# Optimization experiments

Hardware: AMD Instinct MI355X
Metric: run time of the kernel (lower is better)

## Reference

```python
import jax, jax.numpy as jnp
import numpy as np

HEADS = 16
D_MODEL = 1024
D_EXP = 2048  # d_model * expansion_factor
D_HEAD = D_EXP // HEADS
DEPTH = 12
B, L = 2, 2048


def setup_inputs() -> dict:
    key = jax.random.key(0)
    ks = jax.random.split(key, 4)
    x = jax.random.normal(ks[0], (B, L, D_MODEL), dtype=jnp.float32)
    w_in = jax.random.normal(ks[1], (4 * D_EXP, D_MODEL), dtype=jnp.float32) * 0.02
    w_out = jax.random.normal(ks[2], (D_MODEL, D_EXP), dtype=jnp.float32) * (0.02 / np.sqrt(2 * DEPTH))
    # LearnedALiBi init: logspace(0,-6,heads//2,base=2) ++ zeros(heads - heads//2)
    half = HEADS // 2
    slopes = jnp.concatenate([
        jnp.asarray(2.0 ** np.linspace(0.0, -6.0, half), dtype=jnp.float32),
        jnp.zeros((HEADS - half,), dtype=jnp.float32),
    ])
    smear_factor = jnp.linspace(-6.0, 6.0, HEADS, dtype=jnp.float32)
    return {
        "x": x, "w_in": w_in, "w_out": w_out,
        "ln_in_g": jnp.ones((D_MODEL,), jnp.float32), "ln_in_b": jnp.zeros((D_MODEL,), jnp.float32),
        "ln_out_g": jnp.ones((D_MODEL,), jnp.float32), "ln_out_b": jnp.zeros((D_MODEL,), jnp.float32),
        "slopes": slopes, "smear_factor": smear_factor,
    }


def _layernorm(x, g, b, eps=1e-5):
    mu = jnp.mean(x, axis=-1, keepdims=True)
    var = jnp.mean(jnp.square(x - mu), axis=-1, keepdims=True)
    return (x - mu) * jax.lax.rsqrt(var + eps) * g + b


def reference(x, w_in, w_out, ln_in_g, ln_in_b, ln_out_g, ln_out_b, slopes, smear_factor):
    b, l, d = x.shape
    h = _layernorm(x, ln_in_g, ln_in_b)
    qkvp = h @ w_in.T  # (b, l, 4*D_EXP)
    q, k, v, p = jnp.split(qkvp, 4, axis=-1)

    def to_heads(t):  # b i (h d) -> b h i d
        return t.reshape(b, l, HEADS, D_HEAD).transpose(0, 2, 1, 3)

    q, k, v = to_heads(q), to_heads(k), to_heads(v)

    # key smearing: k_i <- (1-s)*k_i + s*k_{i-1}
    smear = jax.nn.sigmoid(smear_factor)[None, :, None, None]
    k_shift = jnp.pad(k, ((0, 0), (0, 0), (1, 0), (0, 0)))[:, :, :-1]
    k = (1.0 - smear) * k + smear * k_shift

    logits = jnp.einsum('bhid,bhjd->bhij', q, k) * (D_HEAD ** -0.5)
    # learned ALiBi bias: j * slope_h  (depends only on key index)
    alibi = jnp.arange(l, dtype=logits.dtype)[None, None, None, :] * slopes[None, :, None, None]
    # causal bias: -1e10 * (1 - tril)
    i_idx = jnp.arange(l)
    causal = jnp.where(i_idx[:, None] >= i_idx[None, :], 0.0, -1e10)[None, None]
    a = jax.nn.softmax(logits + alibi + causal, axis=-1)

    o = jnp.einsum('bhij,bhjd->bhid', a, v)
    o = o.transpose(0, 2, 1, 3).reshape(b, l, D_EXP)  # b h i d -> b i (h d)
    gated = jax.nn.silu(p) * o
    y = gated @ w_out.T
    return _layernorm(y, ln_out_g, ln_out_b)
```

## Files before the change

kernel.cpp:

```cpp
#include <hip/hip_runtime.h>
#include <hip/hip_bf16.h>
#include <stdint.h>


typedef __bf16 bf16;
typedef bf16  bf16x8 __attribute__((ext_vector_type(8)));
typedef bf16  bf16x4 __attribute__((ext_vector_type(4)));
typedef float f32x4  __attribute__((ext_vector_type(4)));

#define SEQ   2048
#define NBATC 2

__device__ __forceinline__ void gld_lds16(const bf16* g, bf16* l) {
  __builtin_amdgcn_global_load_lds((const __attribute__((address_space(1))) void*)g,
                                   (__attribute__((address_space(3))) void*)l, 16, 0, 0);
}

__global__ __launch_bounds__(256) void cvt_kernel(const float* __restrict__ in,
                                                  bf16* __restrict__ out, int n8) {
  int t = blockIdx.x * 256 + threadIdx.x;
  if (t >= n8) return;
  const float4* p = (const float4*)in + (size_t)t * 2;
  float4 a = p[0], b = p[1];
  bf16x8 o;
  o[0] = (bf16)a.x; o[1] = (bf16)a.y; o[2] = (bf16)a.z; o[3] = (bf16)a.w;
  o[4] = (bf16)b.x; o[5] = (bf16)b.y; o[6] = (bf16)b.z; o[7] = (bf16)b.w;
  *((bf16x8*)out + t) = o;
}

template<bool BF16OUT>
__global__ __launch_bounds__(256) void ln_kernel(const float* __restrict__ x,
    const float* __restrict__ gamma, const float* __restrict__ beta,
    void* __restrict__ out) {
  const int row = blockIdx.x;
  const int tid = threadIdx.x;
  float4 v = *(const float4*)(x + (size_t)row * 1024 + tid * 4);
  float s  = v.x + v.y + v.z + v.w;
  float ss = v.x * v.x + v.y * v.y + v.z * v.z + v.w * v.w;
#pragma unroll
  for (int m = 1; m < 64; m <<= 1) { s += __shfl_xor(s, m, 64); ss += __shfl_xor(ss, m, 64); }
  __shared__ float red[8];
  if ((tid & 63) == 0) { red[tid >> 6] = s; red[(tid >> 6) + 4] = ss; }
  __syncthreads();
  s  = red[0] + red[1] + red[2] + red[3];
  ss = red[4] + red[5] + red[6] + red[7];
  const float mu  = s * (1.f / 1024.f);
  const float inv = rsqrtf(ss * (1.f / 1024.f) - mu * mu + 1e-5f);
  float4 g  = *(const float4*)(gamma + tid * 4);
  float4 bb = *(const float4*)(beta  + tid * 4);
  float y0 = (v.x - mu) * inv * g.x + bb.x;
  float y1 = (v.y - mu) * inv * g.y + bb.y;
  float y2 = (v.z - mu) * inv * g.z + bb.z;
  float y3 = (v.w - mu) * inv * g.w + bb.w;
  if (BF16OUT) {
    bf16* o = (bf16*)out + (size_t)row * 1024 + tid * 4;
    o[0] = (bf16)y0; o[1] = (bf16)y1; o[2] = (bf16)y2; o[3] = (bf16)y3;
  } else {
    float* o = (float*)out + (size_t)row * 1024 + tid * 4;
    o[0] = y0; o[1] = y1; o[2] = y2; o[3] = y3;
  }
}

__global__ __launch_bounds__(256) void prep_kernel(const bf16* __restrict__ qkvp,
    const float* __restrict__ smf, bf16* __restrict__ ksm, bf16* __restrict__ vt) {
  __shared__ bf16 T[128][72];
  const int kt = blockIdx.x, bh = blockIdx.y;
  const int b = bh >> 4, h = bh & 15;
  const int t = threadIdx.x;

  {
    int i = t >> 2, d0 = (t & 3) * 32;
    const bf16* src = qkvp + (size_t)(b * SEQ + kt * 64 + i) * 8192 + 4096 + h * 128 + d0;
#pragma unroll
    for (int m = 0; m < 4; m++) {
      bf16x8 v8 = *(const bf16x8*)(src + m * 8);
#pragma unroll
      for (int e = 0; e < 8; e++) T[d0 + m * 8 + e][i] = v8[e];
    }
  }

  {
    float sm = 1.f / (1.f + __expf(-smf[h]));
#pragma unroll
    for (int j = 0; j < 4; j++) {
      int c  = j * 256 + t;
      int il = c >> 4, d8 = c & 15;
      int i  = kt * 64 + il;
      const bf16* base = qkvp + (size_t)(b * SEQ + i) * 8192 + 2048 + h * 128 + d8 * 8;
      bf16x8 cur = *(const bf16x8*)base;
      bf16x8 prv = cur;
      if (i > 0) prv = *(const bf16x8*)(base - 8192);
      bf16x8 o;
#pragma unroll
      for (int e = 0; e < 8; e++) {
        float pv = (i > 0) ? (float)prv[e] : 0.f;
        o[e] = (bf16)((1.f - sm) * (float)cur[e] + sm * pv);
      }
      size_t idx = ((size_t)bh * SEQ + i) * 128 + ((d8 * 8) ^ ((i & 7) << 3));
      *(bf16x8*)(ksm + idx) = o;
    }
  }

  __syncthreads();
  {
    int d = t >> 1, i0 = (t & 1) * 32;
    bf16* dst = vt + (size_t)bh * (SEQ * 128) + (size_t)kt * 8192 + d * 64;
#pragma unroll
    for (int m = 0; m < 4; m++) {
      bf16x8 v8 = *(const bf16x8*)&T[d][i0 + m * 8];
      *(bf16x8*)(dst + (((i0 + m * 8)) ^ ((d & 7) << 3))) = v8;
    }
  }
}

__global__ __launch_bounds__(512, 2) void gemm256(const bf16* __restrict__ A,
    const bf16* __restrict__ Bt, bf16* __restrict__ C, int M, int N, int K,
    int RX, int SX, int SY) {
  __shared__ bf16 As[2][2][128 * 64];
  __shared__ bf16 Bs[2][2][128 * 64];
  const int w   = blockIdx.x;
  const int xcd = w & 7, idx = w >> 3;
  const int rx = xcd % RX, ry = xcd / RX;
  const int bx = rx * SX + idx % SX;
  const int by = ry * SY + idx / SX;
  const int tid  = threadIdx.x;
  const int lane = tid & 63, wid = tid >> 6;
  const int l4 = lane >> 4, l16 = lane & 15;
  const int wr = wid >> 2, wc = wid & 3;
  const int rowBase = by * 256, colBase = bx * 256;
  const int NT = K >> 6;

  f32x4 acc[8][4];
  const f32x4 z = {0.f, 0.f, 0.f, 0.f};
#pragma unroll
  for (int i = 0; i < 8; i++)
#pragma unroll
    for (int j = 0; j < 4; j++) acc[i][j] = z;

  auto stage_pair = [&](int t_, int hp) {
    const int buf = t_ & 1, k0 = t_ * 64;
#pragma unroll
    for (int half = 0; half < 2; ++half) {
      const bf16* src = (hp == 0) ? (A  + (size_t)(rowBase + half * 128) * K)
                                  : (Bt + (size_t)(colBase + half * 128) * K);
      bf16* dst = (hp == 0) ? &As[buf][half][0] : &Bs[buf][half][0];
#pragma unroll
      for (int j = 0; j < 2; ++j) {
        const int c   = j * 512 + tid;
        const int row = c >> 3;
        const int sc  = ((c & 7) * 8) ^ ((row & 7) << 3);
        gld_lds16(src + (size_t)row * K + k0 + sc, dst + c * 8);
      }
    }
  };

  stage_pair(0, 0);
  stage_pair(0, 1);
  asm volatile("s_waitcnt vmcnt(0)" ::: "memory");
  __builtin_amdgcn_sched_barrier(0);
  __builtin_amdgcn_s_barrier();

  for (int t = 0; t < NT; ++t) {
    const int buf = t & 1;
    const bf16* aH = &As[buf][wr][0];
    const bf16* bH = &Bs[buf][wc >> 1][0];
    bf16x8 bfr[4];
#pragma unroll
    for (int p = 0; p < 4; ++p) {
      const int ks = p >> 1, mh = p & 1;
      bf16x8 af[4];
#pragma unroll
      for (int q = 0; q < 4; ++q) {
        const int lr = mh * 64 + q * 16 + l16;
        af[q] = *(const bf16x8*)&aH[lr * 64 + ((ks * 32 + l4 * 8) ^ ((lr & 7) << 3))];
      }
      if (mh == 0) {
#pragma unroll
        for (int ni = 0; ni < 4; ++ni) {
          const int lr = (wc & 1) * 64 + ni * 16 + l16;
          bfr[ni] = *(const bf16x8*)&bH[lr * 64 + ((ks * 32 + l4 * 8) ^ ((lr & 7) << 3))];
        }
      }
      if (p == 0 && t + 1 < NT) stage_pair(t + 1, 0);
      if (p == 1 && t + 1 < NT) stage_pair(t + 1, 1);
      __builtin_amdgcn_s_barrier();
      asm volatile("s_waitcnt lgkmcnt(0)" ::: "memory");
      __builtin_amdgcn_sched_barrier(0);
      __builtin_amdgcn_s_setprio(1);
#pragma unroll
      for (int q = 0; q < 4; ++q)
#pragma unroll
        for (int ni = 0; ni < 4; ++ni)
          acc[mh * 4 + q][ni] =
              __builtin_amdgcn_mfma_f32_16x16x32_bf16(af[q], bfr[ni], acc[mh * 4 + q][ni], 0, 0, 0);
      __builtin_amdgcn_s_setprio(0);
      if (p == 3) {
        asm volatile("s_waitcnt vmcnt(0)" ::: "memory");
        __builtin_amdgcn_sched_barrier(0);
      }
      __builtin_amdgcn_s_barrier();
    }
  }

#pragma unroll
  for (int mi = 0; mi < 8; ++mi)
#pragma unroll
    for (int ni = 0; ni < 4; ++ni) {
      int row = rowBase + wr * 128 + mi * 16 + l4 * 4;
      int col = colBase + wc * 64 + ni * 16 + l16;
#pragma unroll
      for (int r = 0; r < 4; ++r)
        C[(size_t)(row + r) * N + col] = (bf16)acc[mi][ni][r];
    }
}

template<typename OutT>
__global__ __launch_bounds__(256) void gemm_bt(const bf16* __restrict__ A,
    const bf16* __restrict__ Bt, OutT* __restrict__ C, int M, int N, int K,
    int RX, int SX, int SY) {
  __shared__ bf16 As[128 * 32];
  __shared__ bf16 Bs[128 * 32];
  const int w   = blockIdx.x;
  const int xcd = w & 7, idx = w >> 3;
  const int rx = xcd % RX, ry = xcd / RX;
  const int bx = rx * SX + idx % SX;
  const int by = ry * SY + idx / SX;
  const int tid  = threadIdx.x;
  const int lane = tid & 63, wid = tid >> 6;
  const int l4 = lane >> 4, l16 = lane & 15;
  const int wr = wid >> 1, wc = wid & 1;
  const int rowBase = by * 128, colBase = bx * 128;

  const bf16* gA = A  + (size_t)(rowBase + (tid >> 2)) * K + (tid & 3) * 8;
  const bf16* gB = Bt + (size_t)(colBase + (tid >> 2)) * K + (tid & 3) * 8;
  const size_t rowStep = (size_t)64 * K;

  f32x4 acc[4][4];
  const f32x4 z = {0.f, 0.f, 0.f, 0.f};
#pragma unroll
  for (int i = 0; i < 4; i++)
#pragma unroll
    for (int j = 0; j < 4; j++) acc[i][j] = z;

  for (int k0 = 0; k0 < K; k0 += 32) {
    __syncthreads();
    gld_lds16(gA + k0,           &As[tid * 8]);
    gld_lds16(gA + rowStep + k0, &As[2048 + tid * 8]);
    gld_lds16(gB + k0,           &Bs[tid * 8]);
    gld_lds16(gB + rowStep + k0, &Bs[2048 + tid * 8]);
    __syncthreads();
    bf16x8 af[4], bfr[4];
#pragma unroll
    for (int mi = 0; mi < 4; mi++)
      af[mi] = *(const bf16x8*)&As[(wr * 64 + mi * 16 + l16) * 32 + l4 * 8];
#pragma unroll
    for (int ni = 0; ni < 4; ni++)
      bfr[ni] = *(const bf16x8*)&Bs[(wc * 64 + ni * 16 + l16) * 32 + l4 * 8];
#pragma unroll
    for (int mi = 0; mi < 4; mi++)
#pragma unroll
      for (int ni = 0; ni < 4; ni++)
        acc[mi][ni] = __builtin_amdgcn_mfma_f32_16x16x32_bf16(af[mi], bfr[ni], acc[mi][ni], 0, 0, 0);
  }
#pragma unroll
  for (int mi = 0; mi < 4; mi++)
#pragma unroll
    for (int ni = 0; ni < 4; ni++) {
      int row = rowBase + wr * 64 + mi * 16 + l4 * 4;
      int col = colBase + wc * 64 + ni * 16 + l16;
#pragma unroll
      for (int r = 0; r < 4; r++)
        C[(size_t)(row + r) * N + col] = (OutT)acc[mi][ni][r];
    }
}

__global__ __launch_bounds__(512, 2) void attn_kernel(const bf16* __restrict__ qkvp,
    const bf16* __restrict__ ksm, const bf16* __restrict__ vt,
    const float* __restrict__ slopes, bf16* __restrict__ gated) {
  const int w   = blockIdx.x;
  const int xcd = w & 7;
  const int bh  = xcd * 4 + ((w >> 3) & 3);
  const int pr  = w >> 5;
  const int b   = bh >> 4, h = bh & 15;
  const int tid = threadIdx.x, wid = tid >> 6, lane = tid & 63;
  const int l4 = lane >> 4, l16 = lane & 15;
  const int swz = (l16 & 7) << 3;
  const float LOG2E = 1.44269504f;
  const float s2 = 0.08838834764831845f * LOG2E;
  const float slopeL = slopes[h] * LOG2E;

  __shared__ bf16 Kb[4][64 * 128];
  __shared__ bf16 Vb[4][64 * 128];
  __shared__ bf16 P_lds[128 * 64];

  const bf16* ksmB = ksm + (size_t)bh * SEQ * 128;
  const bf16* vtB  = vt  + (size_t)bh * SEQ * 128;

  auto stage = [&](int kt, int bsel) {
#pragma unroll
    for (int j = 0; j < 2; j++) {
      const int c = j * 512 + tid;
      gld_lds16(ksmB + (size_t)kt * 8192 + c * 8, &Kb[bsel][c * 8]);
      gld_lds16(vtB  + (size_t)kt * 8192 + c * 8, &Vb[bsel][c * 8]);
    }
  };

  auto run_strip = [&](int qtile) {
    const int nt = 2 * qtile + 2;
    const int iq = qtile * 128 + wid * 16 + l16;
    bf16x8 qf[4];
    {
      const bf16* qrow = qkvp + (size_t)(b * SEQ + iq) * 8192 + h * 128;
#pragma unroll
      for (int kb = 0; kb < 4; kb++) qf[kb] = *(const bf16x8*)(qrow + kb * 32 + l4 * 8);
    }
    f32x4 oacc[8];
    const f32x4 z = {0.f, 0.f, 0.f, 0.f};
#pragma unroll
    for (int i = 0; i < 8; i++) oacc[i] = z;
    float m2 = -1e38f, lpart = 0.f;

    auto tile = [&](int t, const bf16* K_, const bf16* V_) {
      f32x4 sacc[4];
#pragma unroll
      for (int jf = 0; jf < 4; jf++) {
        f32x4 a = z;
#pragma unroll
        for (int kb = 0; kb < 4; kb++) {
          bf16x8 kf = *(const bf16x8*)&K_[(jf * 16 + l16) * 128 + ((kb * 32 + l4 * 8) ^ swz)];
          a = __builtin_amdgcn_mfma_f32_16x16x32_bf16(kf, qf[kb], a, 0, 0, 0);
        }
        sacc[jf] = a;
      }

      const bool diag = (t >= 2 * qtile);
      const int kbase = t * 64 + l4 * 4;
#pragma unroll
      for (int jf = 0; jf < 4; jf++) {
#pragma unroll
        for (int r = 0; r < 4; r++) {
          int j = kbase + jf * 16 + r;
          float v = fmaf(sacc[jf][r], s2, (float)j * slopeL);
          if (diag && j > iq) v = -1e38f;
          sacc[jf][r] = v;
        }
      }

      float mx = sacc[0][0];
#pragma unroll
      for (int jf = 0; jf < 4; jf++)
#pragma unroll
        for (int r = 0; r < 4; r++) mx = fmaxf(mx, sacc[jf][r]);
      mx = fmaxf(mx, __shfl_xor(mx, 16, 64));
      mx = fmaxf(mx, __shfl_xor(mx, 32, 64));

      if (__any(mx > m2 + 14.f)) {
        float mnew  = fmaxf(m2, mx);
        float alpha = __builtin_amdgcn_exp2f(m2 - mnew);
        m2 = mnew;
        lpart *= alpha;
#pragma unroll
        for (int df = 0; df < 8; df++) oacc[df] *= alpha;
      }

      float rs = 0.f;
#pragma unroll
      for (int jf = 0; jf < 4; jf++) {
        bf16x4 pw;
#pragma unroll
        for (int r = 0; r < 4; r++) {
          float pe = __builtin_amdgcn_exp2f(sacc[jf][r] - m2);
          rs += pe;
          pw[r] = (bf16)pe;
        }
        *(bf16x4*)&P_lds[(wid * 16 + l16) * 64 + ((jf * 16 + l4 * 4) ^ swz)] = pw;
      }
      lpart += rs;

#pragma unroll
      for (int kb2 = 0; kb2 < 2; ++kb2) {
        bf16x8 pf = *(const bf16x8*)&P_lds[(wid * 16 + l16) * 64 + ((kb2 * 32 + l4 * 8) ^ swz)];
#pragma unroll
        for (int df = 0; df < 8; df++) {
          bf16x8 vf = *(const bf16x8*)&V_[(df * 16 + l16) * 64 + ((kb2 * 32 + l4 * 8) ^ swz)];
          oacc[df] = __builtin_amdgcn_mfma_f32_16x16x32_bf16(vf, pf, oacc[df], 0, 0, 0);
        }
      }
    };

    stage(0, 0);
    stage(1, 1);
    for (int tp = 0; tp < nt; tp += 2) {
      if (tp + 2 < nt) {
        stage(tp + 2, (tp + 2) & 3);
        stage(tp + 3, (tp + 3) & 3);
        asm volatile("s_waitcnt vmcnt(8)" ::: "memory");
      } else {
        asm volatile("s_waitcnt vmcnt(0)" ::: "memory");
      }
      __builtin_amdgcn_sched_barrier(0);
      __builtin_amdgcn_s_barrier();
      tile(tp,     Kb[tp & 3],       Vb[tp & 3]);
      tile(tp + 1, Kb[(tp + 1) & 3], Vb[(tp + 1) & 3]);
      asm volatile("s_waitcnt lgkmcnt(0)" ::: "memory");
      __builtin_amdgcn_s_barrier();
    }

    lpart += __shfl_xor(lpart, 16, 64);
    lpart += __shfl_xor(lpart, 32, 64);
    const float linv = 1.f / lpart;
    const bf16* pgrow = qkvp + (size_t)(b * SEQ + iq) * 8192 + 6144 + h * 128;
    bf16* grow = gated + (size_t)(b * SEQ + iq) * 2048 + h * 128;
#pragma unroll
    for (int df = 0; df < 8; df++) {
      const int d0 = df * 16 + l4 * 4;
      bf16x4 pg4 = *(const bf16x4*)(pgrow + d0);
      bf16x4 o4;
#pragma unroll
      for (int r = 0; r < 4; r++) {
        float o  = oacc[df][r] * linv;
        float pg = (float)pg4[r];
        float silu = pg / (1.f + __expf(-pg));
        o4[r] = (bf16)(silu * o);
      }
      *(bf16x4*)(grow + d0) = o4;
    }
  };

  run_strip(15 - pr);
  run_strip(pr);
}

extern "C" void kernel_launch(void* const* d_in, const int* in_sizes, int n_in,
                              void* d_out, int out_size, void* d_ws, size_t ws_size,
                              hipStream_t stream) {
  (void)in_sizes; (void)n_in; (void)out_size; (void)ws_size;
  const float* x      = (const float*)d_in[0];
  const float* w_in   = (const float*)d_in[1];
  const float* w_out  = (const float*)d_in[2];
  const float* lnig   = (const float*)d_in[3];
  const float* lnib   = (const float*)d_in[4];
  const float* lnog   = (const float*)d_in[5];
  const float* lnob   = (const float*)d_in[6];
  const float* slopes = (const float*)d_in[7];
  const float* smf    = (const float*)d_in[8];
  float* out = (float*)d_out;

  char* ws = (char*)d_ws;
  size_t off = 0;
  bf16* hb      = (bf16*)(ws + off); off += (size_t)4096 * 1024 * 2;
  bf16* w_in_b  = (bf16*)(ws + off); off += (size_t)8192 * 1024 * 2;
  bf16* w_out_b = (bf16*)(ws + off); off += (size_t)1024 * 2048 * 2;
  bf16* qkvp    = (bf16*)(ws + off); off += (size_t)4096 * 8192 * 2;
  bf16* ksm     = (bf16*)(ws + off); off += (size_t)32 * 2048 * 128 * 2;
  bf16* gated   = (bf16*)(ws + off); off += (size_t)4096 * 2048 * 2;
  float* yb     = (float*)(ws + off); off += (size_t)4096 * 1024 * 4;
  bf16* vt      = (bf16*)yb;

  cvt_kernel<<<4096, 256, 0, stream>>>(w_in,  w_in_b,  8388608 / 8);
  cvt_kernel<<<1024, 256, 0, stream>>>(w_out, w_out_b, 2097152 / 8);
  ln_kernel<true><<<4096, 256, 0, stream>>>(x, lnig, lnib, hb);
  gemm256<<<512, 512, 0, stream>>>(hb, w_in_b, qkvp, 4096, 8192, 1024, 4, 8, 8);
  prep_kernel<<<dim3(32, 32), 256, 0, stream>>>(qkvp, smf, ksm, vt);
  attn_kernel<<<256, 512, 0, stream>>>(qkvp, ksm, vt, slopes, gated);
  gemm_bt<float><<<256, 256, 0, stream>>>(gated, w_out_b, yb, 4096, 1024, 2048, 1, 8, 4);
  ln_kernel<false><<<4096, 256, 0, stream>>>(yb, lnog, lnob, out);
}
```

Measured before the change: 229.1 us.

## Double-buffer output GEMM, share K/V tiles across attention strips, merge staging

The output projection GEMM is replaced by a double-buffered version with 64-wide K tiles and swizzled LDS, so global loads overlap the MFMA work instead of sitting between syncthreads. The attention kernel now processes its two query strips together, so each K/V tile loaded for the long strip is reused by the short strip rather than streamed twice. The big input GEMM issues both staging halves at the first sub-step. The cost is more registers (two sets of Q fragments and accumulators) and more LDS in the GEMM, which may lower occupancy.

```diff
diff --git a/kernel.cpp b/kernel.cpp
--- a/kernel.cpp
+++ b/kernel.cpp
@@ -181,8 +181,10 @@
           bfr[ni] = *(const bf16x8*)&bH[lr * 64 + ((ks * 32 + l4 * 8) ^ ((lr & 7) << 3))];
         }
       }
-      if (p == 0 && t + 1 < NT) stage_pair(t + 1, 0);
-      if (p == 1 && t + 1 < NT) stage_pair(t + 1, 1);
+      if (p == 0 && t + 1 < NT) {
+        stage_pair(t + 1, 0);
+        stage_pair(t + 1, 1);
+      }
       __builtin_amdgcn_s_barrier();
       asm volatile("s_waitcnt lgkmcnt(0)" ::: "memory");
       __builtin_amdgcn_sched_barrier(0);
@@ -214,12 +216,11 @@
     }
 }
 
-template<typename OutT>
-__global__ __launch_bounds__(256) void gemm_bt(const bf16* __restrict__ A,
-    const bf16* __restrict__ Bt, OutT* __restrict__ C, int M, int N, int K,
+__global__ __launch_bounds__(256, 2) void gemm128(const bf16* __restrict__ A,
+    const bf16* __restrict__ Bt, float* __restrict__ C, int M, int N, int K,
     int RX, int SX, int SY) {
-  __shared__ bf16 As[128 * 32];
-  __shared__ bf16 Bs[128 * 32];
+  __shared__ bf16 As[2][128 * 64];
+  __shared__ bf16 Bs[2][128 * 64];
   const int w   = blockIdx.x;
   const int xcd = w & 7, idx = w >> 3;
   const int rx = xcd % RX, ry = xcd / RX;
@@ -230,10 +231,7 @@
   const int l4 = lane >> 4, l16 = lane & 15;
   const int wr = wid >> 1, wc = wid & 1;
   const int rowBase = by * 128, colBase = bx * 128;
-
-  const bf16* gA = A  + (size_t)(rowBase + (tid >> 2)) * K + (tid & 3) * 8;
-  const bf16* gB = Bt + (size_t)(colBase + (tid >> 2)) * K + (tid & 3) * 8;
-  const size_t rowStep = (size_t)64 * K;
+  const int NT = K >> 6;
 
   f32x4 acc[4][4];
   const f32x4 z = {0.f, 0.f, 0.f, 0.f};
@@ -242,35 +240,61 @@
 #pragma unroll
     for (int j = 0; j < 4; j++) acc[i][j] = z;
 
-  for (int k0 = 0; k0 < K; k0 += 32) {
-    __syncthreads();
-    gld_lds16(gA + k0,           &As[tid * 8]);
-    gld_lds16(gA + rowStep + k0, &As[2048 + tid * 8]);
-    gld_lds16(gB + k0,           &Bs[tid * 8]);
-    gld_lds16(gB + rowStep + k0, &Bs[2048 + tid * 8]);
-    __syncthreads();
-    bf16x8 af[4], bfr[4];
-#pragma unroll
-    for (int mi = 0; mi < 4; mi++)
-      af[mi] = *(const bf16x8*)&As[(wr * 64 + mi * 16 + l16) * 32 + l4 * 8];
-#pragma unroll
-    for (int ni = 0; ni < 4; ni++)
-      bfr[ni] = *(const bf16x8*)&Bs[(wc * 64 + ni * 16 + l16) * 32 + l4 * 8];
-#pragma unroll
-    for (int mi = 0; mi < 4; mi++)
-#pragma unroll
-      for (int ni = 0; ni < 4; ni++)
-        acc[mi][ni] = __builtin_amdgcn_mfma_f32_16x16x32_bf16(af[mi], bfr[ni], acc[mi][ni], 0, 0, 0);
-  }
-#pragma unroll
-  for (int mi = 0; mi < 4; mi++)
-#pragma unroll
-    for (int ni = 0; ni < 4; ni++) {
+  auto stage = [&](int t_, int buf) {
+    const int k0 = t_ * 64;
+#pragma unroll
+    for (int j = 0; j < 4; ++j) {
+      const int c   = j * 256 + tid;
+      const int row = c >> 3;
+      const int sc  = ((c & 7) * 8) ^ ((row & 7) << 3);
+      gld_lds16(A  + (size_t)(rowBase + row) * K + k0 + sc, &As[buf][c * 8]);
+      gld_lds16(Bt + (size_t)(colBase + row) * K + k0 + sc, &Bs[buf][c * 8]);
+    }
+  };
+
+  stage(0, 0);
+  for (int t = 0; t < NT; ++t) {
+    const int cur = t & 1;
+    if (t + 1 < NT) {
+      stage(t + 1, cur ^ 1);
+      asm volatile("s_waitcnt vmcnt(8)" ::: "memory");
+    } else {
+      asm volatile("s_waitcnt vmcnt(0)" ::: "memory");
+    }
+    __builtin_amdgcn_sched_barrier(0);
+    __builtin_amdgcn_s_barrier();
+    const bf16* a_ = &As[cur][0];
+    const bf16* b_ = &Bs[cur][0];
+#pragma unroll
+    for (int ks = 0; ks < 2; ++ks) {
+      bf16x8 bfr[4];
+#pragma unroll
+      for (int ni = 0; ni < 4; ++ni) {
+        const int br = wc * 64 + ni * 16 + l16;
+        bfr[ni] = *(const bf16x8*)&b_[br * 64 + ((ks * 32 + l4 * 8) ^ ((br & 7) << 3))];
+      }
+#pragma unroll
+      for (int mi = 0; mi < 4; ++mi) {
+        const int ar = wr * 64 + mi * 16 + l16;
+        bf16x8 af = *(const bf16x8*)&a_[ar * 64 + ((ks * 32 + l4 * 8) ^ ((ar & 7) << 3))];
+#pragma unroll
+        for (int ni = 0; ni < 4; ++ni)
+          acc[mi][ni] = __builtin_amdgcn_mfma_f32_16x16x32_bf16(af, bfr[ni], acc[mi][ni], 0, 0, 0);
+      }
+    }
+    asm volatile("s_waitcnt lgkmcnt(0)" ::: "memory");
+    __builtin_amdgcn_s_barrier();
+  }
+
+#pragma unroll
+  for (int mi = 0; mi < 4; ++mi)
+#pragma unroll
+    for (int ni = 0; ni < 4; ++ni) {
       int row = rowBase + wr * 64 + mi * 16 + l4 * 4;
       int col = colBase + wc * 64 + ni * 16 + l16;
 #pragma unroll
-      for (int r = 0; r < 4; r++)
-        C[(size_t)(row + r) * N + col] = (OutT)acc[mi][ni][r];
+      for (int r = 0; r < 4; ++r)
+        C[(size_t)(row + r) * N + col] = acc[mi][ni][r];
     }
 }
 
@@ -281,6 +305,9 @@
   const int xcd = w & 7;
   const int bh  = xcd * 4 + ((w >> 3) & 3);
   const int pr  = w >> 5;
+  const int qtA = 15 - pr, qtB = pr;
+  const int ntA = 32 - 2 * pr;
+  const int ntB = 2 * pr + 2;
   const int b   = bh >> 4, h = bh & 15;
   const int tid = threadIdx.x, wid = tid >> 6, lane = tid & 63;
   const int l4 = lane >> 4, l16 = lane & 15;
@@ -305,107 +332,116 @@
     }
   };
 
-  auto run_strip = [&](int qtile) {
-    const int nt = 2 * qtile + 2;
-    const int iq = qtile * 128 + wid * 16 + l16;
-    bf16x8 qf[4];
-    {
-      const bf16* qrow = qkvp + (size_t)(b * SEQ + iq) * 8192 + h * 128;
-#pragma unroll
-      for (int kb = 0; kb < 4; kb++) qf[kb] = *(const bf16x8*)(qrow + kb * 32 + l4 * 8);
-    }
-    f32x4 oacc[8];
-    const f32x4 z = {0.f, 0.f, 0.f, 0.f};
-#pragma unroll
-    for (int i = 0; i < 8; i++) oacc[i] = z;
-    float m2 = -1e38f, lpart = 0.f;
-
-    auto tile = [&](int t, const bf16* K_, const bf16* V_) {
-      f32x4 sacc[4];
-#pragma unroll
-      for (int jf = 0; jf < 4; jf++) {
-        f32x4 a = z;
-#pragma unroll
-        for (int kb = 0; kb < 4; kb++) {
-          bf16x8 kf = *(const bf16x8*)&K_[(jf * 16 + l16) * 128 + ((kb * 32 + l4 * 8) ^ swz)];
-          a = __builtin_amdgcn_mfma_f32_16x16x32_bf16(kf, qf[kb], a, 0, 0, 0);
-        }
-        sacc[jf] = a;
-      }
-
-      const bool diag = (t >= 2 * qtile);
-      const int kbase = t * 64 + l4 * 4;
-#pragma unroll
-      for (int jf = 0; jf < 4; jf++) {
-#pragma unroll
-        for (int r = 0; r < 4; r++) {
-          int j = kbase + jf * 16 + r;
-          float v = fmaf(sacc[jf][r], s2, (float)j * slopeL);
-          if (diag && j > iq) v = -1e38f;
-          sacc[jf][r] = v;
-        }
-      }
-
-      float mx = sacc[0][0];
-#pragma unroll
-      for (int jf = 0; jf < 4; jf++)
-#pragma unroll
-        for (int r = 0; r < 4; r++) mx = fmaxf(mx, sacc[jf][r]);
-      mx = fmaxf(mx, __shfl_xor(mx, 16, 64));
-      mx = fmaxf(mx, __shfl_xor(mx, 32, 64));
-
-      if (__any(mx > m2 + 14.f)) {
-        float mnew  = fmaxf(m2, mx);
-        float alpha = __builtin_amdgcn_exp2f(m2 - mnew);
-        m2 = mnew;
-        lpart *= alpha;
-#pragma unroll
-        for (int df = 0; df < 8; df++) oacc[df] *= alpha;
-      }
-
-      float rs = 0.f;
-#pragma unroll
-      for (int jf = 0; jf < 4; jf++) {
-        bf16x4 pw;
-#pragma unroll
-        for (int r = 0; r < 4; r++) {
-          float pe = __builtin_amdgcn_exp2f(sacc[jf][r] - m2);
-          rs += pe;
-          pw[r] = (bf16)pe;
-        }
-        *(bf16x4*)&P_lds[(wid * 16 + l16) * 64 + ((jf * 16 + l4 * 4) ^ swz)] = pw;
-      }
-      lpart += rs;
-
-#pragma unroll
-      for (int kb2 = 0; kb2 < 2; ++kb2) {
-        bf16x8 pf = *(const bf16x8*)&P_lds[(wid * 16 + l16) * 64 + ((kb2 * 32 + l4 * 8) ^ swz)];
-#pragma unroll
-        for (int df = 0; df < 8; df++) {
-          bf16x8 vf = *(const bf16x8*)&V_[(df * 16 + l16) * 64 + ((kb2 * 32 + l4 * 8) ^ swz)];
-          oacc[df] = __builtin_amdgcn_mfma_f32_16x16x32_bf16(vf, pf, oacc[df], 0, 0, 0);
-        }
-      }
-    };
-
-    stage(0, 0);
-    stage(1, 1);
-    for (int tp = 0; tp < nt; tp += 2) {
-      if (tp + 2 < nt) {
-        stage(tp + 2, (tp + 2) & 3);
-        stage(tp + 3, (tp + 3) & 3);
-        asm volatile("s_waitcnt vmcnt(8)" ::: "memory");
-      } else {
-        asm volatile("s_waitcnt vmcnt(0)" ::: "memory");
-      }
-      __builtin_amdgcn_sched_barrier(0);
-      __builtin_amdgcn_s_barrier();
-      tile(tp,     Kb[tp & 3],       Vb[tp & 3]);
-      tile(tp + 1, Kb[(tp + 1) & 3], Vb[(tp + 1) & 3]);
-      asm volatile("s_waitcnt lgkmcnt(0)" ::: "memory");
-      __builtin_amdgcn_s_barrier();
-    }
-
+  const int iqA = qtA * 128 + wid * 16 + l16;
+  const int iqB = qtB * 128 + wid * 16 + l16;
+  bf16x8 qfA[4], qfB[4];
+  {
+    const bf16* qa = qkvp + (size_t)(b * SEQ + iqA) * 8192 + h * 128;
+    const bf16* qb = qkvp + (size_t)(b * SEQ + iqB) * 8192 + h * 128;
+#pragma unroll
+    for (int kb = 0; kb < 4; kb++) {
+      qfA[kb] = *(const bf16x8*)(qa + kb * 32 + l4 * 8);
+      qfB[kb] = *(const bf16x8*)(qb + kb * 32 + l4 * 8);
+    }
+  }
+  f32x4 oaccA[8], oaccB[8];
+  const f32x4 z = {0.f, 0.f, 0.f, 0.f};
+#pragma unroll
+  for (int i = 0; i < 8; i++) { oaccA[i] = z; oaccB[i] = z; }
+  float m2A = -1e38f, lpA = 0.f, m2B = -1e38f, lpB = 0.f;
+
+  auto tile = [&](int t, int qtile, int iq, bf16x8 (&qf)[4], f32x4 (&oacc)[8],
+                  float& m2, float& lpart, const bf16* K_, const bf16* V_) {
+    f32x4 sacc[4];
+#pragma unroll
+    for (int jf = 0; jf < 4; jf++) {
+      f32x4 a = z;
+#pragma unroll
+      for (int kb = 0; kb < 4; kb++) {
+        bf16x8 kf = *(const bf16x8*)&K_[(jf * 16 + l16) * 128 + ((kb * 32 + l4 * 8) ^ swz)];
+        a = __builtin_amdgcn_mfma_f32_16x16x32_bf16(kf, qf[kb], a, 0, 0, 0);
+      }
+      sacc[jf] = a;
+    }
+
+    const bool diag = (t >= 2 * qtile);
+    const int kbase = t * 64 + l4 * 4;
+#pragma unroll
+    for (int jf = 0; jf < 4; jf++) {
+#pragma unroll
+      for (int r = 0; r < 4; r++) {
+        int j = kbase + jf * 16 + r;
+        float v = fmaf(sacc[jf][r], s2, (float)j * slopeL);
+        if (diag && j > iq) v = -1e38f;
+        sacc[jf][r] = v;
+      }
+    }
+
+    float mx = sacc[0][0];
+#pragma unroll
+    for (int jf = 0; jf < 4; jf++)
+#pragma unroll
+      for (int r = 0; r < 4; r++) mx = fmaxf(mx, sacc[jf][r]);
+    mx = fmaxf(mx, __shfl_xor(mx, 16, 64));
+    mx = fmaxf(mx, __shfl_xor(mx, 32, 64));
+
+    if (__any(mx > m2 + 14.f)) {
+      float mnew  = fmaxf(m2, mx);
+      float alpha = __builtin_amdgcn_exp2f(m2 - mnew);
+      m2 = mnew;
+      lpart *= alpha;
+#pragma unroll
+      for (int df = 0; df < 8; df++) oacc[df] *= alpha;
+    }
+
+    float rs = 0.f;
+#pragma unroll
+    for (int jf = 0; jf < 4; jf++) {
+      bf16x4 pw;
+#pragma unroll
+      for (int r = 0; r < 4; r++) {
+        float pe = __builtin_amdgcn_exp2f(sacc[jf][r] - m2);
+        rs += pe;
+        pw[r] = (bf16)pe;
+      }
+      *(bf16x4*)&P_lds[(wid * 16 + l16) * 64 + ((jf * 16 + l4 * 4) ^ swz)] = pw;
+    }
+    lpart += rs;
+
+#pragma unroll
+    for (int kb2 = 0; kb2 < 2; ++kb2) {
+      bf16x8 pf = *(const bf16x8*)&P_lds[(wid * 16 + l16) * 64 + ((kb2 * 32 + l4 * 8) ^ swz)];
+#pragma unroll
+      for (int df = 0; df < 8; df++) {
+        bf16x8 vf = *(const bf16x8*)&V_[(df * 16 + l16) * 64 + ((kb2 * 32 + l4 * 8) ^ swz)];
+        oacc[df] = __builtin_amdgcn_mfma_f32_16x16x32_bf16(vf, pf, oacc[df], 0, 0, 0);
+      }
+    }
+  };
+
+  stage(0, 0);
+  stage(1, 1);
+  for (int tp = 0; tp < ntA; tp += 2) {
+    if (tp + 2 < ntA) {
+      stage(tp + 2, (tp + 2) & 3);
+      stage(tp + 3, (tp + 3) & 3);
+      asm volatile("s_waitcnt vmcnt(8)" ::: "memory");
+    } else {
+      asm volatile("s_waitcnt vmcnt(0)" ::: "memory");
+    }
+    __builtin_amdgcn_sched_barrier(0);
+    __builtin_amdgcn_s_barrier();
+    tile(tp, qtA, iqA, qfA, oaccA, m2A, lpA, Kb[tp & 3], Vb[tp & 3]);
+    if (tp < ntB)
+      tile(tp, qtB, iqB, qfB, oaccB, m2B, lpB, Kb[tp & 3], Vb[tp & 3]);
+    tile(tp + 1, qtA, iqA, qfA, oaccA, m2A, lpA, Kb[(tp + 1) & 3], Vb[(tp + 1) & 3]);
+    if (tp + 1 < ntB)
+      tile(tp + 1, qtB, iqB, qfB, oaccB, m2B, lpB, Kb[(tp + 1) & 3], Vb[(tp + 1) & 3]);
+    asm volatile("s_waitcnt lgkmcnt(0)" ::: "memory");
+    __builtin_amdgcn_s_barrier();
+  }
+
+  auto epi = [&](int iq, f32x4 (&oacc)[8], float lpart) {
     lpart += __shfl_xor(lpart, 16, 64);
     lpart += __shfl_xor(lpart, 32, 64);
     const float linv = 1.f / lpart;
@@ -426,9 +462,8 @@
       *(bf16x4*)(grow + d0) = o4;
     }
   };
-
-  run_strip(15 - pr);
-  run_strip(pr);
+  epi(iqA, oaccA, lpA);
+  epi(iqB, oaccB, lpB);
 }
 
 extern "C" void kernel_launch(void* const* d_in, const int* in_sizes, int n_in,
@@ -463,6 +498,6 @@
   gemm256<<<512, 512, 0, stream>>>(hb, w_in_b, qkvp, 4096, 8192, 1024, 4, 8, 8);
   prep_kernel<<<dim3(32, 32), 256, 0, stream>>>(qkvp, smf, ksm, vt);
   attn_kernel<<<256, 512, 0, stream>>>(qkvp, ksm, vt, slopes, gated);
-  gemm_bt<float><<<256, 256, 0, stream>>>(gated, w_out_b, yb, 4096, 1024, 2048, 1, 8, 4);
+  gemm128<<<256, 256, 0, stream>>>(gated, w_out_b, yb, 4096, 1024, 2048, 1, 8, 4);
   ln_kernel<false><<<4096, 256, 0, stream>>>(yb, lnog, lnob, out);
 }
```

New measurement: 332.8 us. +45.3%, slower.
